# Performance work log

Measured on AMD Instinct MI355X. Metric: run time of the kernel, lower is better.

The kernel has to match this reference:

```python
import jax, jax.numpy as jnp
import numpy as np

NT = 100000   # total word nodes (B graphs * N nodes)
B = 50        # number of graphs in the batch
E = 1600000   # total edges
V = 15000     # vocab (num_word)
D_IN = 128    # h_inp
D_H = 128     # h_dim


def setup_inputs() -> dict:
    key = jax.random.key(0)
    ks = jax.random.split(key, 12)
    return {
        "node_ids": jax.random.randint(ks[0], (NT,), 0, V),
        "src": jax.random.randint(ks[1], (E,), 0, NT),
        "dst": jax.random.randint(ks[2], (E,), 0, NT),
        "edge_weight": jax.random.uniform(ks[3], (E,), dtype=jnp.float32),
        "y_data": jax.random.uniform(ks[4], (B,), dtype=jnp.float32),
        "word_embeds": jax.random.normal(ks[5], (V, D_IN), dtype=jnp.float32) * 0.1,
        "W1": jax.random.normal(ks[6], (D_IN, D_H), dtype=jnp.float32) * 0.05,
        "b1": jax.random.normal(ks[7], (D_H,), dtype=jnp.float32) * 0.05,
        "W2": jax.random.normal(ks[8], (D_H, D_H), dtype=jnp.float32) * 0.05,
        "b2": jax.random.normal(ks[9], (D_H,), dtype=jnp.float32) * 0.05,
        "W_out": jax.random.normal(ks[10], (D_H, 1), dtype=jnp.float32) * 0.05,
        "b_out": jax.random.normal(ks[11], (1,), dtype=jnp.float32) * 0.05,
    }


def _word_graph_layer(h, W, b, src, dst, edge_weight, deg):
    # Linear projection, then DGL u_mul_e + mean aggregation over incoming edges.
    Wh = h @ W + b                                   # [NT, D]
    m = Wh[src] * edge_weight[:, None]               # gather + edge-weight mul, [E, D]
    s = jax.ops.segment_sum(m, dst, num_segments=NT)  # scatter-add, [NT, D]
    # mean over incoming messages; nodes with no in-edges keep 0 (DGL semantics)
    return jnp.where(deg[:, None] > 0, s / jnp.maximum(deg, 1.0)[:, None], 0.0)


def reference(node_ids, src, dst, edge_weight, y_data, word_embeds,
              W1, b1, W2, b2, W_out, b_out):
    deg = jax.ops.segment_sum(jnp.ones_like(edge_weight), dst, num_segments=NT)
    h = word_embeds[node_ids]                        # [NT, D_IN]
    h = _word_graph_layer(h, W1, b1, src, dst, edge_weight, deg)
    h = jax.nn.leaky_relu(h, negative_slope=0.01)
    h = _word_graph_layer(h, W2, b2, src, dst, edge_weight, deg)
    # per-graph mean pool; equal graph sizes so padded mean == true mean
    word_pool = h.reshape(B, NT // B, D_H).mean(axis=1)   # [B, D_H]
    logits = (word_pool @ W_out + b_out).reshape(-1)      # [B]
    # binary_cross_entropy_with_logits, mean reduction (numerically stable)
    loss = jnp.mean(jnp.maximum(logits, 0.0) - logits * y_data
                    + jnp.log1p(jnp.exp(-jnp.abs(logits))))
    y_pred = jax.nn.sigmoid(logits)[:, None]              # [B, 1]
    return (loss, y_pred)
```

## Files before the change

### kernel.cpp

```cpp
#include <hip/hip_runtime.h>
#include <hip/hip_fp16.h>
#include <math.h>

#define NT 100000
#define B_GRAPHS 50
#define NE 1600000
#define V 15000
#define D 128
#define NODES_PER_GRAPH (NT / B_GRAPHS)

#define POOL_N (B_GRAPHS * D + B_GRAPHS)

#define BSH 8
#define BIN_DSTS 256
#define NBIN ((NT + BIN_DSTS - 1) / BIN_DSTS)
#define SLACK (3 * BIN_DSTS)
#define EPB 4096
#define NFB ((NE + EPB - 1) / EPB)
#define BUF_SORT 5632
#define STAGE_STRIDE 4608
#define PAY_STRIDE (STAGE_STRIDE + SLACK)
#define PAY_TAIL 512
#define PR 16
#define PROJ_BLOCKS ((V + PR - 1) / PR)

__device__ __forceinline__ unsigned enc2_e5m2(float a, float b) {
  unsigned ha = __half_as_ushort(__float2half(a));
  unsigned hb = __half_as_ushort(__float2half(b));
  ha = ((ha + 0x7fu + ((ha >> 8) & 1u)) >> 8) & 0xffu;
  hb = ((hb + 0x7fu + ((hb >> 8) & 1u)) >> 8) & 0xffu;
  return ha | (hb << 8);
}
__device__ __forceinline__ unsigned enc4_e5m2(float a, float b, float c, float d) {
  return enc2_e5m2(a, b) | (enc2_e5m2(c, d) << 16);
}

__global__ __launch_bounds__(512)
void k_pb(const float* __restrict__ embeds, const float* __restrict__ W1,
          const float* __restrict__ b1, unsigned* __restrict__ P1p8,
          float* __restrict__ pool, int2* __restrict__ payTail,
          const int* __restrict__ src, const int* __restrict__ dst,
          const float* __restrict__ ew, const int* __restrict__ node_ids,
          int* __restrict__ binCursor, int2* __restrict__ stage) {
  __shared__ union {
    struct {
      int h[512], sc[512], gbase[512], cur[512];
      int wsum[8], woff[8];
      unsigned short binOf[EPB];
      int2 buf[EPB];
    } f;
    struct {
      float sE[PR][D];
      float sO[PR][D];
    } p;
  } U;
  int t = threadIdx.x;
  if (blockIdx.x < NFB) {
    int lane = t & 63, wv = t >> 6;
    U.f.h[t] = 0;
    __syncthreads();
    int base = blockIdx.x * EPB;
    int d_[EPB / 512], b_[EPB / 512];
#pragma unroll
    for (int i = 0; i < EPB / 512; ++i) {
      int e = base + i * 512 + t;
      int d = (e < NE) ? dst[e] : -1;
      d_[i] = d;
      b_[i] = (d >= 0) ? (d >> BSH) : -1;
      if (d >= 0) atomicAdd(&U.f.h[b_[i]], 1);
    }
    __syncthreads();
    int c = U.f.h[t];
    int v = c;
#pragma unroll
    for (int off = 1; off < 64; off <<= 1) {
      int x = __shfl_up(v, off);
      if (lane >= off) v += x;
    }
    if (lane == 63) U.f.wsum[wv] = v;
    __syncthreads();
    if (t == 0) {
      int a = 0;
#pragma unroll
      for (int i = 0; i < 8; ++i) { U.f.woff[i] = a; a += U.f.wsum[i]; }
    }
    __syncthreads();
    int incl = v + U.f.woff[wv];
    U.f.sc[t] = incl;
    U.f.cur[t] = incl - c;
    if (t < NBIN && c > 0) U.f.gbase[t] = atomicAdd(&binCursor[t], c);
    __syncthreads();
    int total = U.f.sc[511];
#pragma unroll
    for (int i = 0; i < EPB / 512; ++i) {
      int e = base + i * 512 + t;
      if (e < NE) {
        int s = src[e];
        unsigned uw = __float_as_uint(ew[e]);
        unsigned wb = (uw + 0x7fffu + ((uw >> 16) & 1u)) & 0xffff0000u;
        int wid = node_ids[s];
        int dl = d_[i] & (BIN_DSTS - 1);
        int p = atomicAdd(&U.f.cur[b_[i]], 1);
        U.f.buf[p] = make_int2((int)(wb | (unsigned)wid), s | (dl << 17));
        U.f.binOf[p] = (unsigned short)b_[i];
      }
    }
    __syncthreads();
    for (int i = t; i < total; i += 512) {
      int b = U.f.binOf[i];
      int local = i - (U.f.sc[b] - U.f.h[b]);
      stage[(size_t)b * STAGE_STRIDE + U.f.gbase[b] + local] = U.f.buf[i];
    }
  } else {
    int pb = blockIdx.x - NFB;
    if (pb == 0) {
      for (int i = t; i < POOL_N; i += 512) pool[i] = 0.f;
      for (int i = t; i < PAY_TAIL; i += 512) payTail[i] = make_int2(0, 0);
    }
    int row0 = pb * PR;
    for (int i = t; i < PR * D; i += 512) {
      int r = i >> 7, c = i & 127;
      int vv = row0 + r;
      U.p.sE[r][c] = (vv < V) ? embeds[(size_t)vv * D + c] : 0.f;
    }
    __syncthreads();
    int c = t & 127, rg = (t >> 7) * 4;
    float bd = b1[c];
    float acc[4];
#pragma unroll
    for (int r = 0; r < 4; ++r) acc[r] = bd;
#pragma unroll 4
    for (int k = 0; k < D; ++k) {
      float w = W1[k * D + c];
#pragma unroll
      for (int r = 0; r < 4; ++r) acc[r] = fmaf(U.p.sE[rg + r][k], w, acc[r]);
    }
#pragma unroll
    for (int r = 0; r < 4; ++r) U.p.sO[rg + r][c] = acc[r];
    __syncthreads();
    {
      int r = t >> 5, li = t & 31;
      int vv = row0 + r;
      if (vv < V)
        P1p8[(size_t)vv * 32 + li] =
            enc4_e5m2(U.p.sO[r][4 * li], U.p.sO[r][4 * li + 1],
                      U.p.sO[r][4 * li + 2], U.p.sO[r][4 * li + 3]);
    }
  }
}

__global__ __launch_bounds__(512)
void k_binsort(const int2* __restrict__ stage, const int* __restrict__ binCnt,
               int* __restrict__ rowD, int* __restrict__ cntD,
               int2* __restrict__ pay) {
  __shared__ int h2[BIN_DSTS], cur2[BIN_DSTS];
  __shared__ float invD[BIN_DSTS];
  __shared__ int wsum4[4], woff4[4];
  __shared__ int sh_end;
  __shared__ int2 buf[BUF_SORT];
  int b = blockIdx.x, t = threadIdx.x;
  int lane = t & 63, wv = t >> 6;
  int cnt = binCnt[b];
  int sb = b * STAGE_STRIDE;
  int pb = b * PAY_STRIDE;
  int dst0 = b << BSH;
  if (t < BIN_DSTS) h2[t] = 0;
  __syncthreads();
  for (int i = t; i < cnt; i += 512)
    atomicAdd(&h2[(stage[sb + i].y >> 17) & 255], 1);
  __syncthreads();
  int c = (t < BIN_DSTS) ? h2[t] : 0;
  int pc = (c + 3) & ~3;
  int v = (t < BIN_DSTS) ? pc : 0;
#pragma unroll
  for (int off = 1; off < 64; off <<= 1) {
    int x = __shfl_up(v, off);
    if (lane >= off) v += x;
  }
  if (lane == 63 && wv < 4) wsum4[wv] = v;
  __syncthreads();
  if (t == 0) {
    int a = 0;
#pragma unroll
    for (int i = 0; i < 4; ++i) { woff4[i] = a; a += wsum4[i]; }
    sh_end = a;
  }
  __syncthreads();
  if (t < BIN_DSTS) {
    int myoff = v + woff4[wv] - pc;
    invD[t] = (c > 0) ? (1.0f / (float)c) : 0.0f;
    cur2[t] = myoff;
    int n = dst0 + t;
    if (n < NT) { rowD[n] = pb + myoff; cntD[n] = c; }
  }
  __syncthreads();
  int end = sh_end + 24;
  if (end > PAY_STRIDE) end = PAY_STRIDE;
  for (int i = t; i < end; i += 512) buf[i] = make_int2(0, 0);
  __syncthreads();
  for (int i = t; i < cnt; i += 512) {
    int2 r = stage[sb + i];
    int dl = (r.y >> 17) & 255;
    float w = __uint_as_float((unsigned)r.x & 0xffff0000u);
    float wp = w * invD[dl];
    unsigned wh = (unsigned)__half_as_ushort(__float2half(wp));
    int p = atomicAdd(&cur2[dl], 1);
    buf[p] = make_int2((int)((wh << 16) | ((unsigned)r.x & 0xffffu)), r.y & 0x1ffff);
  }
  __syncthreads();
  for (int i = t; i < end; i += 512) pay[pb + i] = buf[i];
}

template<bool USE_WID>
__device__ __forceinline__ int pick_idx(const int4& q, int half) {
  int lo = USE_WID ? (q.x & 0xffff) : q.y;
  int hi = USE_WID ? (q.z & 0xffff) : q.w;
  return half ? hi : lo;
}
__device__ __forceinline__ void consume2h(const int4& q, unsigned v, int half,
                                          __half2& A01, __half2& A23, __half2& SW) {
  unsigned wm = (unsigned)(half ? q.z : q.x);
  unsigned wd = (wm >> 16) | (wm & 0xffff0000u);
  unsigned hp0 = ((v & 0xffu) << 8) | ((v & 0xff00u) << 16);
  unsigned hp1 = ((v >> 8) & 0xff00u) | (v & 0xff000000u);
  __half2 w2 = *(__half2*)&wd;
  A01 = __hfma2(w2, *(__half2*)&hp0, A01);
  A23 = __hfma2(w2, *(__half2*)&hp1, A23);
  SW = __hadd2(SW, w2);
}

template<bool USE_WID>
__device__ __forceinline__ void gather_row(const int2* __restrict__ pay,
                                           const unsigned* __restrict__ tab,
                                           int beg, int cnt, int li, int half,
                                           __half2& A01, __half2& A23, __half2& SW) {
  int G = (cnt + 3) >> 2;
  const int4* __restrict__ pp = (const int4*)(pay + beg);
  int4 q0a = pp[0], q0b = pp[1];
  int4 q1a = pp[2], q1b = pp[3];
  int4 q2a = pp[4], q2b = pp[5];
  int4 q3a = pp[6], q3b = pp[7];
  int4 q4a = pp[8], q4b = pp[9];
  unsigned va0 = tab[(size_t)pick_idx<USE_WID>(q0a, half) * 32 + li];
  unsigned vb0 = tab[(size_t)pick_idx<USE_WID>(q0b, half) * 32 + li];
  unsigned va1 = tab[(size_t)pick_idx<USE_WID>(q1a, half) * 32 + li];
  unsigned vb1 = tab[(size_t)pick_idx<USE_WID>(q1b, half) * 32 + li];
  unsigned va2 = tab[(size_t)pick_idx<USE_WID>(q2a, half) * 32 + li];
  unsigned vb2 = tab[(size_t)pick_idx<USE_WID>(q2b, half) * 32 + li];
  for (int g = 0; g < G; ++g) {
    unsigned vn0 = tab[(size_t)pick_idx<USE_WID>(q3a, half) * 32 + li];
    unsigned vn1 = tab[(size_t)pick_idx<USE_WID>(q3b, half) * 32 + li];
    int4 qna = pp[2 * g + 10];
    int4 qnb = pp[2 * g + 11];
    consume2h(q0a, va0, half, A01, A23, SW);
    consume2h(q0b, vb0, half, A01, A23, SW);
    q0a = q1a; q0b = q1b; q1a = q2a; q1b = q2b; q2a = q3a; q2b = q3b;
    q3a = q4a; q3b = q4b; q4a = qna; q4b = qnb;
    va0 = va1; vb0 = vb1; va1 = va2; vb1 = vb2; va2 = vn0; vb2 = vn1;
  }
}

#define NPW1 10
__global__ void k_agg1(const int2* __restrict__ pay,
                       const int* __restrict__ rowD, const int* __restrict__ cntD,
                       const unsigned* __restrict__ P1p8,
                       unsigned* __restrict__ h1p8) {
  int w = threadIdx.x >> 6, lane = threadIdx.x & 63;
  int li = lane & 31, half = lane >> 5;
  int nbase = blockIdx.x * (4 * NPW1) + w * NPW1;
  for (int i = 0; i < NPW1; ++i) {
    int n = nbase + i;
    int beg = __builtin_amdgcn_readfirstlane(rowD[n]);
    int cnt = __builtin_amdgcn_readfirstlane(cntD[n]);
    __half2 A01 = __half2half2(__float2half(0.f));
    __half2 A23 = A01, SW = A01;
    gather_row<true>(pay, P1p8, beg, cnt, li, half, A01, A23, SW);
    float2 f01 = __half22float2(A01);
    float2 f23 = __half22float2(A23);
    float a0 = f01.x, a1 = f01.y, a2 = f23.x, a3 = f23.y;
    a0 += __shfl_down(a0, 32);
    a1 += __shfl_down(a1, 32);
    a2 += __shfl_down(a2, 32);
    a3 += __shfl_down(a3, 32);
    if (lane < 32) {
      float x0 = a0, x1 = a1, x2 = a2, x3 = a3;
      x0 = (x0 > 0.f) ? x0 : 0.01f * x0;
      x1 = (x1 > 0.f) ? x1 : 0.01f * x1;
      x2 = (x2 > 0.f) ? x2 : 0.01f * x2;
      x3 = (x3 > 0.f) ? x3 : 0.01f * x3;
      h1p8[(size_t)n * 32 + li] = enc4_e5m2(x0, x1, x2, x3);
    }
  }
}

#define NPW2 10
#define BLKS_PER_G (NODES_PER_GRAPH / (4 * NPW2))
__global__ void k_agg2(const int2* __restrict__ pay,
                       const int* __restrict__ rowD, const int* __restrict__ cntD,
                       const unsigned* __restrict__ h1p8,
                       float* __restrict__ pool) {
  int g = blockIdx.x / BLKS_PER_G;
  int chunk = blockIdx.x % BLKS_PER_G;
  int w = threadIdx.x >> 6, lane = threadIdx.x & 63;
  int li = lane & 31, half = lane >> 5;
  int nbase = g * NODES_PER_GRAPH + chunk * (4 * NPW2) + w * NPW2;
  __half2 A01 = __half2half2(__float2half(0.f));
  __half2 A23 = A01, SW = A01;
  for (int i = 0; i < NPW2; ++i) {
    int n = nbase + i;
    int beg = __builtin_amdgcn_readfirstlane(rowD[n]);
    int cnt = __builtin_amdgcn_readfirstlane(cntD[n]);
    gather_row<false>(pay, h1p8, beg, cnt, li, half, A01, A23, SW);
  }
  float2 f01 = __half22float2(A01);
  float2 f23 = __half22float2(A23);
  float s0 = f01.x, s1 = f01.y, s2 = f23.x, s3 = f23.y;
  float sc = __low2float(SW);
  s0 += __shfl_down(s0, 32);
  s1 += __shfl_down(s1, 32);
  s2 += __shfl_down(s2, 32);
  s3 += __shfl_down(s3, 32);
  sc += __shfl_down(sc, 32);
  __shared__ float sS[4 * 128];
  __shared__ float sC[4];
  if (lane < 32) {
    sS[w * 128 + 4 * li + 0] = s0;
    sS[w * 128 + 4 * li + 1] = s1;
    sS[w * 128 + 4 * li + 2] = s2;
    sS[w * 128 + 4 * li + 3] = s3;
  }
  if (lane == 0) sC[w] = sc;
  __syncthreads();
  int t = threadIdx.x;
  if (t < 128) {
    float v = sS[t] + sS[128 + t] + sS[256 + t] + sS[384 + t];
    atomicAdd(&pool[g * D + t], v);
  }
  if (t == 0) atomicAdd(&pool[B_GRAPHS * D + g], sC[0] + sC[1] + sC[2] + sC[3]);
}

__global__ void k_final(const float* __restrict__ poolS, const float* __restrict__ poolC,
                        const float* __restrict__ W2, const float* __restrict__ b2,
                        const float* __restrict__ W_out, const float* __restrict__ b_out,
                        const float* __restrict__ y, float* __restrict__ out) {
  __shared__ float w2o[D];
  __shared__ float s2oArr[D];
  __shared__ float s2o_sh;
  __shared__ float logits[64];
  int t = threadIdx.x;
  int w = t >> 6, lane = t & 63;
  if (t < D) {
    float acc = 0.f;
    for (int d = 0; d < D; ++d) acc = fmaf(W2[t * D + d], W_out[d], acc);
    w2o[t] = acc;
  } else {
    int j = t - D;
    s2oArr[j] = b2[j] * W_out[j];
  }
  __syncthreads();
  if (t < 64) {
    float v = s2oArr[lane] + s2oArr[64 + lane];
#pragma unroll
    for (int off = 32; off > 0; off >>= 1) v += __shfl_down(v, off);
    if (lane == 0) s2o_sh = v;
  }
  __syncthreads();
  float s2o = s2o_sh;
  float bout = b_out[0];
  const float invN = 1.0f / (float)NODES_PER_GRAPH;
  for (int g = w; g < B_GRAPHS; g += 4) {
    float v = poolS[g * D + lane] * w2o[lane]
            + poolS[g * D + 64 + lane] * w2o[64 + lane];
#pragma unroll
    for (int off = 32; off > 0; off >>= 1) v += __shfl_down(v, off);
    if (lane == 0) {
      float l = v * invN + poolC[g] * invN * s2o + bout;
      logits[g] = l;
      out[1 + g] = 1.0f / (1.0f + expf(-l));
    }
  }
  __syncthreads();
  if (t < 64) {
    float term = 0.f;
    if (lane < B_GRAPHS) {
      float l = logits[lane];
      term = fmaxf(l, 0.f) - l * y[lane] + log1pf(expf(-fabsf(l)));
    }
#pragma unroll
    for (int off = 32; off > 0; off >>= 1) term += __shfl_down(term, off);
    if (lane == 0) out[0] = term / (float)B_GRAPHS;
  }
}

extern "C" void kernel_launch(void* const* d_in, const int* in_sizes, int n_in,
                              void* d_out, int out_size, void* d_ws, size_t ws_size,
                              hipStream_t stream) {
  const int*   node_ids = (const int*)d_in[0];
  const int*   src      = (const int*)d_in[1];
  const int*   dst      = (const int*)d_in[2];
  const float* ew       = (const float*)d_in[3];
  const float* y        = (const float*)d_in[4];
  const float* embeds   = (const float*)d_in[5];
  const float* W1       = (const float*)d_in[6];
  const float* b1       = (const float*)d_in[7];
  const float* W2       = (const float*)d_in[8];
  const float* b2       = (const float*)d_in[9];
  const float* W_out    = (const float*)d_in[10];
  const float* b_out    = (const float*)d_in[11];
  float* out = (float*)d_out;
  (void)in_sizes; (void)n_in; (void)out_size; (void)ws_size;

  char* ws = (char*)d_ws;
  size_t off = 0;
  auto alloc = [&](size_t bytes) {
    size_t r = off;
    off = (off + bytes + 511) & ~(size_t)511;
    return r;
  };
  size_t o_binCur = alloc(512 * 4);
  size_t o_pool   = alloc((size_t)POOL_N * 4);
  size_t o_rowD   = alloc((size_t)(NT + 1) * 4);
  size_t o_cntD   = alloc((size_t)NT * 4);
  size_t o_P1p8   = alloc((size_t)V * 32 * 4);
  size_t o_h1p8   = alloc((size_t)NT * 32 * 4);
  size_t o_stage  = alloc((size_t)NBIN * STAGE_STRIDE * 8);
  size_t o_pay    = alloc(((size_t)NBIN * PAY_STRIDE + PAY_TAIL) * 8);

  int*      binCursor= (int*)(ws + o_binCur);
  float*    pool     = (float*)(ws + o_pool);
  int*      rowD     = (int*)(ws + o_rowD);
  int*      cntD     = (int*)(ws + o_cntD);
  unsigned* P1p8     = (unsigned*)(ws + o_P1p8);
  unsigned* h1p8     = (unsigned*)(ws + o_h1p8);
  int2*     stage    = (int2*)(ws + o_stage);
  int2*     pay      = (int2*)(ws + o_pay);
  int2*     payTail  = pay + (size_t)NBIN * PAY_STRIDE;

  hipMemsetAsync(binCursor, 0, 512 * 4, stream);
  k_pb<<<NFB + PROJ_BLOCKS, 512, 0, stream>>>(embeds, W1, b1, P1p8, pool, payTail,
                                              src, dst, ew, node_ids, binCursor, stage);
  k_binsort<<<NBIN, 512, 0, stream>>>(stage, binCursor, rowD, cntD, pay);
  k_agg1<<<NT / (4 * NPW1), 256, 0, stream>>>(pay, rowD, cntD, P1p8, h1p8);
  k_agg2<<<B_GRAPHS * BLKS_PER_G, 256, 0, stream>>>(pay, rowD, cntD, h1p8, pool);
  k_final<<<1, 256, 0, stream>>>(pool, pool + B_GRAPHS * D, W2, b2, W_out, b_out, y, out);
}
```

Baseline: 253.7 us.

## Hold bin records in registers and deepen gather prefetch pipeline

The bin-sort kernel now loads each staged edge record once into registers (up to 9 per thread) and reuses it for both the histogram and the scatter. It drops the 45KB shared-memory sort buffer and writes the payload straight to global memory, zeroing the padded region first. This removes a second global read of the stage array and frees LDS for occupancy, but trades it for scattered global writes. The gather loop prefetches one more group of payload entries and table values, which hides latency better at the cost of more registers. The zeroed tail padding is widened to cover the deeper prefetch.

```diff
diff --git a/kernel.cpp b/kernel.cpp
--- a/kernel.cpp
+++ b/kernel.cpp
@@ -17,12 +17,12 @@
 #define SLACK (3 * BIN_DSTS)
 #define EPB 4096
 #define NFB ((NE + EPB - 1) / EPB)
-#define BUF_SORT 5632
 #define STAGE_STRIDE 4608
 #define PAY_STRIDE (STAGE_STRIDE + SLACK)
 #define PAY_TAIL 512
 #define PR 16
 #define PROJ_BLOCKS ((V + PR - 1) / PR)
+#define RPT 9
 
 __device__ __forceinline__ unsigned enc2_e5m2(float a, float b) {
   unsigned ha = __half_as_ushort(__float2half(a));
@@ -157,7 +157,6 @@
   __shared__ float invD[BIN_DSTS];
   __shared__ int wsum4[4], woff4[4];
   __shared__ int sh_end;
-  __shared__ int2 buf[BUF_SORT];
   int b = blockIdx.x, t = threadIdx.x;
   int lane = t & 63, wv = t >> 6;
   int cnt = binCnt[b];
@@ -166,8 +165,19 @@
   int dst0 = b << BSH;
   if (t < BIN_DSTS) h2[t] = 0;
   __syncthreads();
-  for (int i = t; i < cnt; i += 512)
-    atomicAdd(&h2[(stage[sb + i].y >> 17) & 255], 1);
+  int2 rec[RPT];
+  int dl_[RPT];
+#pragma unroll
+  for (int k = 0; k < RPT; ++k) {
+    int i = t + k * 512;
+    if (i < cnt) {
+      rec[k] = stage[sb + i];
+      dl_[k] = (rec[k].y >> 17) & 255;
+      atomicAdd(&h2[dl_[k]], 1);
+    } else {
+      dl_[k] = -1;
+    }
+  }
   __syncthreads();
   int c = (t < BIN_DSTS) ? h2[t] : 0;
   int pc = (c + 3) & ~3;
@@ -194,21 +204,21 @@
     if (n < NT) { rowD[n] = pb + myoff; cntD[n] = c; }
   }
   __syncthreads();
-  int end = sh_end + 24;
+  int end = sh_end + 32;
   if (end > PAY_STRIDE) end = PAY_STRIDE;
-  for (int i = t; i < end; i += 512) buf[i] = make_int2(0, 0);
-  __syncthreads();
-  for (int i = t; i < cnt; i += 512) {
-    int2 r = stage[sb + i];
-    int dl = (r.y >> 17) & 255;
-    float w = __uint_as_float((unsigned)r.x & 0xffff0000u);
-    float wp = w * invD[dl];
-    unsigned wh = (unsigned)__half_as_ushort(__float2half(wp));
-    int p = atomicAdd(&cur2[dl], 1);
-    buf[p] = make_int2((int)((wh << 16) | ((unsigned)r.x & 0xffffu)), r.y & 0x1ffff);
-  }
-  __syncthreads();
-  for (int i = t; i < end; i += 512) pay[pb + i] = buf[i];
+  for (int i = t; i < end; i += 512) pay[pb + i] = make_int2(0, 0);
+  __syncthreads();
+#pragma unroll
+  for (int k = 0; k < RPT; ++k) {
+    if (dl_[k] >= 0) {
+      float w = __uint_as_float((unsigned)rec[k].x & 0xffff0000u);
+      float wp = w * invD[dl_[k]];
+      unsigned wh = (unsigned)__half_as_ushort(__float2half(wp));
+      int p = atomicAdd(&cur2[dl_[k]], 1);
+      pay[pb + p] = make_int2((int)((wh << 16) | ((unsigned)rec[k].x & 0xffffu)),
+                              rec[k].y & 0x1ffff);
+    }
+  }
 }
 
 template<bool USE_WID>
@@ -236,27 +246,31 @@
                                            __half2& A01, __half2& A23, __half2& SW) {
   int G = (cnt + 3) >> 2;
   const int4* __restrict__ pp = (const int4*)(pay + beg);
-  int4 q0a = pp[0], q0b = pp[1];
-  int4 q1a = pp[2], q1b = pp[3];
-  int4 q2a = pp[4], q2b = pp[5];
-  int4 q3a = pp[6], q3b = pp[7];
-  int4 q4a = pp[8], q4b = pp[9];
+  int4 q0a = pp[0],  q0b = pp[1];
+  int4 q1a = pp[2],  q1b = pp[3];
+  int4 q2a = pp[4],  q2b = pp[5];
+  int4 q3a = pp[6],  q3b = pp[7];
+  int4 q4a = pp[8],  q4b = pp[9];
+  int4 q5a = pp[10], q5b = pp[11];
   unsigned va0 = tab[(size_t)pick_idx<USE_WID>(q0a, half) * 32 + li];
   unsigned vb0 = tab[(size_t)pick_idx<USE_WID>(q0b, half) * 32 + li];
   unsigned va1 = tab[(size_t)pick_idx<USE_WID>(q1a, half) * 32 + li];
   unsigned vb1 = tab[(size_t)pick_idx<USE_WID>(q1b, half) * 32 + li];
   unsigned va2 = tab[(size_t)pick_idx<USE_WID>(q2a, half) * 32 + li];
   unsigned vb2 = tab[(size_t)pick_idx<USE_WID>(q2b, half) * 32 + li];
+  unsigned va3 = tab[(size_t)pick_idx<USE_WID>(q3a, half) * 32 + li];
+  unsigned vb3 = tab[(size_t)pick_idx<USE_WID>(q3b, half) * 32 + li];
   for (int g = 0; g < G; ++g) {
-    unsigned vn0 = tab[(size_t)pick_idx<USE_WID>(q3a, half) * 32 + li];
-    unsigned vn1 = tab[(size_t)pick_idx<USE_WID>(q3b, half) * 32 + li];
-    int4 qna = pp[2 * g + 10];
-    int4 qnb = pp[2 * g + 11];
+    unsigned vn0 = tab[(size_t)pick_idx<USE_WID>(q4a, half) * 32 + li];
+    unsigned vn1 = tab[(size_t)pick_idx<USE_WID>(q4b, half) * 32 + li];
+    int4 qna = pp[2 * g + 12];
+    int4 qnb = pp[2 * g + 13];
     consume2h(q0a, va0, half, A01, A23, SW);
     consume2h(q0b, vb0, half, A01, A23, SW);
     q0a = q1a; q0b = q1b; q1a = q2a; q1b = q2b; q2a = q3a; q2b = q3b;
-    q3a = q4a; q3b = q4b; q4a = qna; q4b = qnb;
-    va0 = va1; vb0 = vb1; va1 = va2; vb1 = vb2; va2 = vn0; vb2 = vn1;
+    q3a = q4a; q3b = q4b; q4a = q5a; q4b = q5b; q5a = qna; q5b = qnb;
+    va0 = va1; vb0 = vb1; va1 = va2; vb1 = vb2; va2 = va3; vb2 = vb3;
+    va3 = vn0; vb3 = vn1;
   }
 }
 
```

Result: no change. 257.9 us (+1.6%).
